# Kernel tuning notes

Measured on AMD Instinct MI355X. Metric: run time of the kernel, lower is better.

## Reference

```python
import jax, jax.numpy as jnp
import numpy as np
import math

NUM_LABELS = 8
D_MODEL = 1024
NUM_HEADS = 16
D_PADDED = math.ceil(D_MODEL / NUM_HEADS) * NUM_HEADS  # 1024
D_HEAD = D_PADDED // NUM_HEADS  # 64
B, N = 4, 2048


def setup_inputs() -> dict:
    key = jax.random.key(0)
    ks = jax.random.split(key, 7)
    X = jax.random.normal(ks[0], (B, N, D_MODEL), dtype=jnp.float32)
    L = jax.random.randint(ks[1], (B, N), 0, NUM_LABELS, dtype=jnp.int32)
    # per-label QKV linear params (stored as x @ W + b layout)
    s_in = 1.0 / math.sqrt(D_MODEL)
    Wqkv = jax.random.uniform(ks[2], (NUM_LABELS, D_MODEL, 3 * D_PADDED), jnp.float32, -s_in, s_in)
    bqkv = jax.random.uniform(ks[3], (NUM_LABELS, 3 * D_PADDED), jnp.float32, -s_in, s_in)
    s_p = 1.0 / math.sqrt(D_PADDED)
    Wproj = jax.random.uniform(ks[4], (D_PADDED, D_MODEL), jnp.float32, -s_p, s_p)
    bproj = jax.random.uniform(ks[5], (D_MODEL,), jnp.float32, -s_p, s_p)
    return {"X": X, "L": L, "Wqkv": Wqkv, "bqkv": bqkv, "Wproj": Wproj, "bproj": bproj}


def reference(X, L, Wqkv, bqkv, Wproj, bproj):
    Bb, Nn, _ = X.shape
    # Per-label dense QKV projection, routed by label mask (matches original
    # per-label loop; X_masked zeroing is a no-op on selected positions).
    qkv = jnp.zeros((Bb, Nn, 3 * D_PADDED), dtype=X.dtype)
    for l in range(NUM_LABELS):
        m = (L == l)[..., None]  # [B, N, 1]
        qkv_l = jnp.einsum('bnd,do->bno', X, Wqkv[l]) + bqkv[l]
        qkv = jnp.where(m, qkv_l, qkv)
    q, k, v = jnp.split(qkv, 3, axis=-1)
    # [B, H, N, Dh]
    q = q.reshape(Bb, Nn, NUM_HEADS, D_HEAD).transpose(0, 2, 1, 3)
    k = k.reshape(Bb, Nn, NUM_HEADS, D_HEAD).transpose(0, 2, 1, 3)
    v = v.reshape(Bb, Nn, NUM_HEADS, D_HEAD).transpose(0, 2, 1, 3)
    scores = jnp.einsum('bhnd,bhmd->bhnm', q, k) / math.sqrt(D_HEAD)
    probs = jax.nn.softmax(scores, axis=-1)
    out = jnp.einsum('bhnm,bhmd->bhnd', probs, v)
    out = out.transpose(0, 2, 1, 3).reshape(Bb, Nn, D_PADDED)
    return jnp.einsum('bnd,do->bno', out, Wproj) + bproj
```

## Files before the change

kernel.cpp:

```cpp
#include <hip/hip_runtime.h>
#include <math.h>

#define BATCH 4
#define SEQ   2048
#define TOK   (BATCH * SEQ)
#define DM    1024
#define DP    1024
#define NH    16
#define DH    64
#define NLAB  8
#define QKV_C 3072
#define PADL  1152
#define PROWS (NLAB * PADL)
#define GP    72

typedef __attribute__((ext_vector_type(8))) short bf16x8;
typedef __attribute__((ext_vector_type(4))) float f32x4;

__device__ __forceinline__ short f2bf(float f) {
  union { float f; unsigned u; } v; v.f = f;
  unsigned r = v.u + 0x7FFF + ((v.u >> 16) & 1);
  return (short)(r >> 16);
}

__device__ __forceinline__ unsigned cvt_pk_bf16(float lo, float hi) {
  unsigned r;
  asm("v_cvt_pk_bf16_f32 %0, %1, %2" : "=v"(r) : "v"(lo), "v"(hi));
  return r;
}

__device__ __forceinline__ float fast_exp2(float x) {
#if __has_builtin(__builtin_amdgcn_exp2f)
  return __builtin_amdgcn_exp2f(x);
#else
  return exp2f(x);
#endif
}

__global__ void build_lists_k(const int* __restrict__ L, int* __restrict__ sorted,
                              int* __restrict__ rowmap) {
  __shared__ int cnt[NLAB], off[NLAB], cur[NLAB];
  int tid = threadIdx.x;
  if (tid < NLAB) cnt[tid] = 0;
  __syncthreads();
  for (int i = tid; i < TOK; i += 256) atomicAdd(&cnt[L[i]], 1);
  __syncthreads();
  if (tid == 0) {
    int o = 0;
    for (int l = 0; l < NLAB; ++l) { off[l] = o; cur[l] = o; o += cnt[l]; }
  }
  __syncthreads();
  for (int i = tid; i < TOK; i += 256) {
    int l = L[i];
    sorted[atomicAdd(&cur[l], 1)] = i;
  }
  __threadfence();
  __syncthreads();
  for (int p = tid; p < PROWS; p += 256) {
    int l = p / PADL, i = p - l * PADL;
    rowmap[p] = (i < cnt[l]) ? sorted[off[l] + i] : -1;
  }
}

__global__ __launch_bounds__(256) void wt_k(const float* __restrict__ src,
                                            short* __restrict__ dst,
                                            int K, int N) {
  __shared__ float Ts[64][65];
  int m = blockIdx.z;
  src += (size_t)m * K * N;
  dst += (size_t)m * (size_t)N * K;
  int n0 = blockIdx.x * 64, k0 = blockIdx.y * 64;
  int tid = threadIdx.x;
  int r = tid >> 4;
  int c = (tid & 15) << 2;
  #pragma unroll
  for (int it = 0; it < 4; ++it) {
    float4 v = *(const float4*)(src + (size_t)(k0 + r + it * 16) * N + n0 + c);
    Ts[c + 0][r + it * 16] = v.x;
    Ts[c + 1][r + it * 16] = v.y;
    Ts[c + 2][r + it * 16] = v.z;
    Ts[c + 3][r + it * 16] = v.w;
  }
  __syncthreads();
  int n = tid >> 2, ks = (tid & 3) << 4;
  short tmp[16];
  #pragma unroll
  for (int j = 0; j < 16; ++j) tmp[j] = f2bf(Ts[n][ks + j]);
  *(bf16x8*)(dst + (size_t)(n0 + n) * K + k0 + ks)     = *(bf16x8*)&tmp[0];
  *(bf16x8*)(dst + (size_t)(n0 + n) * K + k0 + ks + 8) = *(bf16x8*)&tmp[8];
}

__global__ __launch_bounds__(256) void qkv_mfma_k(
    const float* __restrict__ X, const short* __restrict__ Wt,
    const float* __restrict__ bqkv, const int* __restrict__ rowmap,
    short* __restrict__ qkvb) {
  __shared__ short As[128 * GP];
  __shared__ short Bs[128 * GP];
  int bx = blockIdx.x, by = blockIdx.y;
  int lab = by / 9;
  int pr0 = by * 128;
  int n0  = bx * 128;
  const short* W = Wt + (size_t)lab * QKV_C * DM;

  int tid  = threadIdx.x;
  int lane = tid & 63, w = tid >> 6;
  int wm = w >> 1, wn = w & 1;
  int col = lane & 15, quad = lane >> 4;

  int srow = tid >> 2;
  int scol = (tid & 3) << 4;

  int tokA0 = rowmap[pr0 + srow];
  int tokA1 = rowmap[pr0 + 64 + srow];
  const float* xr0 = (tokA0 >= 0) ? (X + (size_t)tokA0 * DM) : nullptr;
  const float* xr1 = (tokA1 >= 0) ? (X + (size_t)tokA1 * DM) : nullptr;

  f32x4 acc[4][4];
  #pragma unroll
  for (int mi = 0; mi < 4; ++mi)
    #pragma unroll
    for (int ni = 0; ni < 4; ++ni) acc[mi][ni] = (f32x4){0.f, 0.f, 0.f, 0.f};

  for (int k0 = 0; k0 < DM; k0 += 64) {
    #pragma unroll
    for (int rep = 0; rep < 2; ++rep) {
      const float* xr = rep ? xr1 : xr0;
      int row = srow + rep * 64;
      short tmp[16];
      if (xr) {
        #pragma unroll
        for (int q4 = 0; q4 < 4; ++q4) {
          float4 v = *(const float4*)(xr + k0 + scol + q4 * 4);
          tmp[q4 * 4 + 0] = f2bf(v.x);
          tmp[q4 * 4 + 1] = f2bf(v.y);
          tmp[q4 * 4 + 2] = f2bf(v.z);
          tmp[q4 * 4 + 3] = f2bf(v.w);
        }
      } else {
        #pragma unroll
        for (int j = 0; j < 16; ++j) tmp[j] = 0;
      }
      *(bf16x8*)&As[row * GP + scol]     = *(bf16x8*)&tmp[0];
      *(bf16x8*)&As[row * GP + scol + 8] = *(bf16x8*)&tmp[8];
    }
    #pragma unroll
    for (int rep = 0; rep < 2; ++rep) {
      int row = srow + rep * 64;
      const short* wsrc = W + (size_t)(n0 + row) * DM + k0 + scol;
      *(bf16x8*)&Bs[row * GP + scol]     = *(const bf16x8*)(wsrc);
      *(bf16x8*)&Bs[row * GP + scol + 8] = *(const bf16x8*)(wsrc + 8);
    }
    __syncthreads();
    #pragma unroll
    for (int ks = 0; ks < 2; ++ks) {
      bf16x8 a[4], b[4];
      #pragma unroll
      for (int mi = 0; mi < 4; ++mi)
        a[mi] = *(bf16x8*)&As[(wm * 64 + mi * 16 + col) * GP + ks * 32 + (quad << 3)];
      #pragma unroll
      for (int ni = 0; ni < 4; ++ni)
        b[ni] = *(bf16x8*)&Bs[(wn * 64 + ni * 16 + col) * GP + ks * 32 + (quad << 3)];
      #pragma unroll
      for (int mi = 0; mi < 4; ++mi)
        #pragma unroll
        for (int ni = 0; ni < 4; ++ni)
          acc[mi][ni] = __builtin_amdgcn_mfma_f32_16x16x32_bf16(a[mi], b[ni], acc[mi][ni], 0, 0, 0);
    }
    __syncthreads();
  }

  float scale = (bx < 8) ? (0.125f * 1.44269504f) : 1.0f;
  const float* bias = bqkv + lab * QKV_C;
  #pragma unroll
  for (int mi = 0; mi < 4; ++mi) {
    #pragma unroll
    for (int r = 0; r < 4; ++r) {
      int prow = pr0 + wm * 64 + mi * 16 + (quad << 2) + r;
      int t2 = rowmap[prow];
      if (t2 < 0) continue;
      #pragma unroll
      for (int ni = 0; ni < 4; ++ni) {
        int gn = n0 + wn * 64 + ni * 16 + col;
        float v = (acc[mi][ni][r] + bias[gn]) * scale;
        qkvb[(size_t)t2 * QKV_C + gn] = f2bf(v);
      }
    }
  }
}

__global__ __launch_bounds__(256) void vtb_k(const short* __restrict__ qkvb,
                                             short* __restrict__ VTg) {
  __shared__ short T[64 * GP];
  int n0 = blockIdx.x * 64, h = blockIdx.y, b = blockIdx.z;
  int tid = threadIdx.x;
  int r = tid >> 2, cb = tid & 3;
  {
    const short* src = qkvb + ((size_t)(b * SEQ + n0 + r)) * QKV_C + 2 * DP + h * DH + (cb << 4);
    int scc = ((cb + (r >> 4)) & 3) << 4;
    *(bf16x8*)&T[r * GP + scc]     = *(const bf16x8*)(src);
    *(bf16x8*)&T[r * GP + scc + 8] = *(const bf16x8*)(src + 8);
  }
  __syncthreads();
  int d = tid >> 2, nc = (tid & 3) << 4;
  int sc2 = (((d >> 4) + (nc >> 4)) & 3) << 4;
  short tmp[16];
  #pragma unroll
  for (int j = 0; j < 16; ++j) tmp[j] = T[(nc + j) * GP + sc2 + (d & 15)];
  short* dst = VTg + ((size_t)(b * NH + h) * DH + d) * SEQ + n0 + nc;
  *(bf16x8*)&dst[0] = *(bf16x8*)&tmp[0];
  *(bf16x8*)&dst[8] = *(bf16x8*)&tmp[8];
}

__global__ __launch_bounds__(256) void attn_k(short* __restrict__ qkvb,
                                              const short* __restrict__ VTg) {
  int qt = blockIdx.x, h = blockIdx.y, b = blockIdx.z;
  __shared__ short Ks[64 * GP];
  __shared__ short VT[64 * GP];
  __shared__ short Ps[128 * GP];

  int tid  = threadIdx.x;
  int lane = tid & 63;
  int w    = tid >> 6;
  int col  = lane & 15;
  int quad = lane >> 4;

  size_t rowbase = (size_t)b * SEQ;
  int hoff = h * DH;
  int sr = tid >> 2;
  int sc = (tid & 3) << 4;

  const short* ksrc = qkvb + (rowbase + sr) * QKV_C + DP + hoff + sc;
  const short* vsrc = VTg + ((size_t)(b * NH + h) * DH + sr) * SEQ + sc;

  bf16x8 qf0[2], qf1[2];
  {
    const short* q0 = qkvb + (rowbase + qt * 128 + (w << 4) + col) * QKV_C + hoff + (quad << 3);
    const short* q1 = q0 + (size_t)64 * QKV_C;
    qf0[0] = *(const bf16x8*)(q0);
    qf0[1] = *(const bf16x8*)(q0 + 32);
    qf1[0] = *(const bf16x8*)(q1);
    qf1[1] = *(const bf16x8*)(q1 + 32);
  }

  {
    bf16x8 ka = *(const bf16x8*)(ksrc);
    bf16x8 kb = *(const bf16x8*)(ksrc + 8);
    bf16x8 va = *(const bf16x8*)(vsrc);
    bf16x8 vb = *(const bf16x8*)(vsrc + 8);
    *(bf16x8*)&Ks[sr * GP + sc]     = ka;
    *(bf16x8*)&Ks[sr * GP + sc + 8] = kb;
    *(bf16x8*)&VT[sr * GP + sc]     = va;
    *(bf16x8*)&VT[sr * GP + sc + 8] = vb;
  }
  __syncthreads();

  float m_0 = -1e30f, l_0 = 0.f, m_1 = -1e30f, l_1 = 0.f;
  f32x4 o0[4], o1[4];
  #pragma unroll
  for (int nd = 0; nd < 4; ++nd) {
    o0[nd] = (f32x4){0.f, 0.f, 0.f, 0.f};
    o1[nd] = (f32x4){0.f, 0.f, 0.f, 0.f};
  }

  short* ps0 = &Ps[((w << 4) + col) * GP];
  short* ps1 = &Ps[(64 + (w << 4) + col) * GP];

  auto softmax_strip = [&](f32x4* s, float& m_, float& l_, f32x4* o, short* psrow) {
    f32x4 t0, t1;
    #pragma unroll
    for (int i = 0; i < 4; ++i) { t0[i] = fmaxf(s[0][i], s[1][i]); t1[i] = fmaxf(s[2][i], s[3][i]); }
    #pragma unroll
    for (int i = 0; i < 4; ++i) t0[i] = fmaxf(t0[i], t1[i]);
    float mx = fmaxf(fmaxf(t0[0], t0[1]), fmaxf(t0[2], t0[3]));
    mx = fmaxf(mx, __shfl_xor(mx, 16));
    mx = fmaxf(mx, __shfl_xor(mx, 32));
    float mnew  = fmaxf(m_, mx);
    float alpha = fast_exp2(m_ - mnew);
    float p[4][4];
    #pragma unroll
    for (int nj = 0; nj < 4; ++nj)
      #pragma unroll
      for (int r = 0; r < 4; ++r) p[nj][r] = fast_exp2(s[nj][r] - mnew);
    float rs = 0.f;
    #pragma unroll
    for (int nj = 0; nj < 4; ++nj)
      rs += (p[nj][0] + p[nj][1]) + (p[nj][2] + p[nj][3]);
    rs += __shfl_xor(rs, 16);
    rs += __shfl_xor(rs, 32);
    l_ = l_ * alpha + rs;
    m_ = mnew;
    #pragma unroll
    for (int nd = 0; nd < 4; ++nd)
      #pragma unroll
      for (int r = 0; r < 4; ++r) o[nd][r] *= alpha;
    #pragma unroll
    for (int nj = 0; nj < 4; ++nj) {
      uint2 u;
      u.x = cvt_pk_bf16(p[nj][0], p[nj][1]);
      u.y = cvt_pk_bf16(p[nj][2], p[nj][3]);
      *(uint2*)&psrow[nj * 16 + (quad << 2)] = u;
    }
  };

  auto compute_tile = [&]() {
    f32x4 s0[4], s1[4];
    #pragma unroll
    for (int nj = 0; nj < 4; ++nj) {
      s0[nj] = (f32x4){0.f, 0.f, 0.f, 0.f};
      s1[nj] = (f32x4){0.f, 0.f, 0.f, 0.f};
    }
    #pragma unroll
    for (int ks = 0; ks < 2; ++ks) {
      #pragma unroll
      for (int nj = 0; nj < 4; ++nj) {
        bf16x8 aK = *(bf16x8*)&Ks[((nj << 4) + col) * GP + (ks << 5) + (quad << 3)];
        s0[nj] = __builtin_amdgcn_mfma_f32_16x16x32_bf16(aK, qf0[ks], s0[nj], 0, 0, 0);
        s1[nj] = __builtin_amdgcn_mfma_f32_16x16x32_bf16(aK, qf1[ks], s1[nj], 0, 0, 0);
      }
    }
    softmax_strip(s0, m_0, l_0, o0, ps0);
    softmax_strip(s1, m_1, l_1, o1, ps1);
    #pragma unroll
    for (int ks = 0; ks < 2; ++ks) {
      bf16x8 bP0 = *(bf16x8*)&ps0[(ks << 5) + (quad << 3)];
      bf16x8 bP1 = *(bf16x8*)&ps1[(ks << 5) + (quad << 3)];
      #pragma unroll
      for (int nd = 0; nd < 4; ++nd) {
        bf16x8 aV = *(bf16x8*)&VT[((nd << 4) + col) * GP + (ks << 5) + (quad << 3)];
        o0[nd] = __builtin_amdgcn_mfma_f32_16x16x32_bf16(aV, bP0, o0[nd], 0, 0, 0);
        o1[nd] = __builtin_amdgcn_mfma_f32_16x16x32_bf16(aV, bP1, o1[nd], 0, 0, 0);
      }
    }
  };

  for (int kt = 0; kt < SEQ / 64 - 1; ++kt) {
    const short* kn = ksrc + (size_t)(kt + 1) * 64 * QKV_C;
    const short* vn = vsrc + (size_t)(kt + 1) * 64;
    bf16x8 ka = *(const bf16x8*)(kn);
    bf16x8 kb = *(const bf16x8*)(kn + 8);
    bf16x8 va = *(const bf16x8*)(vn);
    bf16x8 vb = *(const bf16x8*)(vn + 8);

    compute_tile();
    __syncthreads();
    *(bf16x8*)&Ks[sr * GP + sc]     = ka;
    *(bf16x8*)&Ks[sr * GP + sc + 8] = kb;
    *(bf16x8*)&VT[sr * GP + sc]     = va;
    *(bf16x8*)&VT[sr * GP + sc + 8] = vb;
    __syncthreads();
  }
  compute_tile();

  #pragma unroll
  for (int s = 0; s < 2; ++s) {
    float inv = 1.f / (s ? l_1 : l_0);
    f32x4* o = s ? o1 : o0;
    size_t row = rowbase + qt * 128 + s * 64 + (w << 4) + col;
    #pragma unroll
    for (int nd = 0; nd < 4; ++nd) {
      uint2 u;
      u.x = cvt_pk_bf16(o[nd][0] * inv, o[nd][1] * inv);
      u.y = cvt_pk_bf16(o[nd][2] * inv, o[nd][3] * inv);
      *(uint2*)(qkvb + row * QKV_C + hoff + (nd << 4) + (quad << 2)) = u;
    }
  }
}

__global__ __launch_bounds__(256) void proj_mfma_k(
    const short* __restrict__ Ab, const short* __restrict__ Wt,
    const float* __restrict__ bias, float* __restrict__ out) {
  __shared__ short As[128 * GP];
  __shared__ short Bs[128 * GP];
  int n0 = blockIdx.x * 128, m0 = blockIdx.y * 128;

  int tid  = threadIdx.x;
  int lane = tid & 63, w = tid >> 6;
  int wm = w >> 1, wn = w & 1;
  int col = lane & 15, quad = lane >> 4;
  int srow = tid >> 2;
  int scol = (tid & 3) << 4;

  f32x4 acc[4][4];
  #pragma unroll
  for (int mi = 0; mi < 4; ++mi)
    #pragma unroll
    for (int ni = 0; ni < 4; ++ni) acc[mi][ni] = (f32x4){0.f, 0.f, 0.f, 0.f};

  for (int k0 = 0; k0 < DP; k0 += 64) {
    #pragma unroll
    for (int rep = 0; rep < 2; ++rep) {
      int row = srow + rep * 64;
      const short* asrc = Ab + (size_t)(m0 + row) * QKV_C + k0 + scol;
      *(bf16x8*)&As[row * GP + scol]     = *(const bf16x8*)(asrc);
      *(bf16x8*)&As[row * GP + scol + 8] = *(const bf16x8*)(asrc + 8);
      const short* wsrc = Wt + (size_t)(n0 + row) * DP + k0 + scol;
      *(bf16x8*)&Bs[row * GP + scol]     = *(const bf16x8*)(wsrc);
      *(bf16x8*)&Bs[row * GP + scol + 8] = *(const bf16x8*)(wsrc + 8);
    }
    __syncthreads();
    #pragma unroll
    for (int ks = 0; ks < 2; ++ks) {
      bf16x8 a[4], b[4];
      #pragma unroll
      for (int mi = 0; mi < 4; ++mi)
        a[mi] = *(bf16x8*)&As[(wm * 64 + mi * 16 + col) * GP + ks * 32 + (quad << 3)];
      #pragma unroll
      for (int ni = 0; ni < 4; ++ni)
        b[ni] = *(bf16x8*)&Bs[(wn * 64 + ni * 16 + col) * GP + ks * 32 + (quad << 3)];
      #pragma unroll
      for (int mi = 0; mi < 4; ++mi)
        #pragma unroll
        for (int ni = 0; ni < 4; ++ni)
          acc[mi][ni] = __builtin_amdgcn_mfma_f32_16x16x32_bf16(a[mi], b[ni], acc[mi][ni], 0, 0, 0);
    }
    __syncthreads();
  }

  #pragma unroll
  for (int mi = 0; mi < 4; ++mi) {
    #pragma unroll
    for (int r = 0; r < 4; ++r) {
      int m = m0 + wm * 64 + mi * 16 + (quad << 2) + r;
      #pragma unroll
      for (int ni = 0; ni < 4; ++ni) {
        int gn = n0 + wn * 64 + ni * 16 + col;
        out[(size_t)m * DM + gn] = acc[mi][ni][r] + bias[gn];
      }
    }
  }
}

extern "C" void kernel_launch(void* const* d_in, const int* in_sizes, int n_in,
                              void* d_out, int out_size, void* d_ws, size_t ws_size,
                              hipStream_t stream) {
  (void)in_sizes; (void)n_in; (void)out_size; (void)ws_size;
  const float* X     = (const float*)d_in[0];
  const int*   L     = (const int*)d_in[1];
  const float* Wqkv  = (const float*)d_in[2];
  const float* bqkv  = (const float*)d_in[3];
  const float* Wproj = (const float*)d_in[4];
  const float* bproj = (const float*)d_in[5];
  float* out = (float*)d_out;

  char* ws = (char*)d_ws;
  short* qkvb    = (short*)ws;
  short* Wqkv_t  = (short*)(ws + (size_t)TOK * QKV_C * 2);
  short* Wproj_t = (short*)(ws + (size_t)TOK * QKV_C * 2
                               + (size_t)NLAB * QKV_C * DM * 2);
  int* sorted = (int*)((char*)Wproj_t + (size_t)DP * DM * 2);
  int* rowmap = sorted + TOK;
  short* VTg = Wqkv_t;

  build_lists_k<<<dim3(1), dim3(256), 0, stream>>>(L, sorted, rowmap);
  wt_k<<<dim3(QKV_C / 64, DM / 64, NLAB), dim3(256), 0, stream>>>(Wqkv, Wqkv_t, DM, QKV_C);
  wt_k<<<dim3(DM / 64, DP / 64, 1), dim3(256), 0, stream>>>(Wproj, Wproj_t, DP, DM);
  qkv_mfma_k<<<dim3(QKV_C / 128, PROWS / 128), dim3(256), 0, stream>>>(
      X, Wqkv_t, bqkv, rowmap, qkvb);
  vtb_k<<<dim3(SEQ / 64, NH, BATCH), dim3(256), 0, stream>>>(qkvb, VTg);
  attn_k<<<dim3(SEQ / 128, NH, BATCH), dim3(256), 0, stream>>>(qkvb, VTg);
  proj_mfma_k<<<dim3(DM / 128, TOK / 128), dim3(256), 0, stream>>>(
      qkvb, Wproj_t, bproj, out);
}
```

Measured before the change: 542.5 us.

## Pre-gather X to bf16 and register-prefetch next K tile in GEMMs

Adds a gather kernel that writes label-sorted X rows as bf16 into a padded buffer, so the QKV GEMM no longer does per-tile fp32 loads, bf16 conversion and row indirection repeated across 24 column blocks. Both the QKV and projection GEMMs now prefetch the next K tile into registers after the barrier, so global loads overlap the MFMA work. The cost is an extra kernel launch, an extra bf16 buffer in the workspace, and higher register pressure.

Result: faster. 476.9 us (-12.1%).

```diff
diff --git a/kernel.cpp b/kernel.cpp
--- a/kernel.cpp
+++ b/kernel.cpp
@@ -62,6 +62,23 @@
   }
 }
 
+__global__ __launch_bounds__(256) void xg_k(const float* __restrict__ X,
+                                            const int* __restrict__ rowmap,
+                                            short* __restrict__ Xg) {
+  int p = blockIdx.x;
+  int t = rowmap[p];
+  int c = threadIdx.x << 2;
+  short* dst = Xg + (size_t)p * DM + c;
+  if (t >= 0) {
+    float4 v = *(const float4*)(X + (size_t)t * DM + c);
+    short tmp[4] = { f2bf(v.x), f2bf(v.y), f2bf(v.z), f2bf(v.w) };
+    *(uint2*)dst = *(uint2*)tmp;
+  } else {
+    uint2 z; z.x = 0u; z.y = 0u;
+    *(uint2*)dst = z;
+  }
+}
+
 __global__ __launch_bounds__(256) void wt_k(const float* __restrict__ src,
                                             short* __restrict__ dst,
                                             int K, int N) {
@@ -91,7 +108,7 @@
 }
 
 __global__ __launch_bounds__(256) void qkv_mfma_k(
-    const float* __restrict__ X, const short* __restrict__ Wt,
+    const short* __restrict__ Xg, const short* __restrict__ Wt,
     const float* __restrict__ bqkv, const int* __restrict__ rowmap,
     short* __restrict__ qkvb) {
   __shared__ short As[128 * GP];
@@ -110,10 +127,10 @@
   int srow = tid >> 2;
   int scol = (tid & 3) << 4;
 
-  int tokA0 = rowmap[pr0 + srow];
-  int tokA1 = rowmap[pr0 + 64 + srow];
-  const float* xr0 = (tokA0 >= 0) ? (X + (size_t)tokA0 * DM) : nullptr;
-  const float* xr1 = (tokA1 >= 0) ? (X + (size_t)tokA1 * DM) : nullptr;
+  const short* a0 = Xg + (size_t)(pr0 + srow) * DM + scol;
+  const short* a1 = Xg + (size_t)(pr0 + 64 + srow) * DM + scol;
+  const short* b0 = W + (size_t)(n0 + srow) * DM + scol;
+  const short* b1 = W + (size_t)(n0 + 64 + srow) * DM + scol;
 
   f32x4 acc[4][4];
   #pragma unroll
@@ -121,36 +138,29 @@
     #pragma unroll
     for (int ni = 0; ni < 4; ++ni) acc[mi][ni] = (f32x4){0.f, 0.f, 0.f, 0.f};
 
+  bf16x8 ra[4], rb[4];
+  ra[0] = *(const bf16x8*)(a0);     ra[1] = *(const bf16x8*)(a0 + 8);
+  ra[2] = *(const bf16x8*)(a1);     ra[3] = *(const bf16x8*)(a1 + 8);
+  rb[0] = *(const bf16x8*)(b0);     rb[1] = *(const bf16x8*)(b0 + 8);
+  rb[2] = *(const bf16x8*)(b1);     rb[3] = *(const bf16x8*)(b1 + 8);
+
   for (int k0 = 0; k0 < DM; k0 += 64) {
-    #pragma unroll
-    for (int rep = 0; rep < 2; ++rep) {
-      const float* xr = rep ? xr1 : xr0;
-      int row = srow + rep * 64;
-      short tmp[16];
-      if (xr) {
-        #pragma unroll
-        for (int q4 = 0; q4 < 4; ++q4) {
-          float4 v = *(const float4*)(xr + k0 + scol + q4 * 4);
-          tmp[q4 * 4 + 0] = f2bf(v.x);
-          tmp[q4 * 4 + 1] = f2bf(v.y);
-          tmp[q4 * 4 + 2] = f2bf(v.z);
-          tmp[q4 * 4 + 3] = f2bf(v.w);
-        }
-      } else {
-        #pragma unroll
-        for (int j = 0; j < 16; ++j) tmp[j] = 0;
-      }
-      *(bf16x8*)&As[row * GP + scol]     = *(bf16x8*)&tmp[0];
-      *(bf16x8*)&As[row * GP + scol + 8] = *(bf16x8*)&tmp[8];
-    }
-    #pragma unroll
-    for (int rep = 0; rep < 2; ++rep) {
-      int row = srow + rep * 64;
-      const short* wsrc = W + (size_t)(n0 + row) * DM + k0 + scol;
-      *(bf16x8*)&Bs[row * GP + scol]     = *(const bf16x8*)(wsrc);
-      *(bf16x8*)&Bs[row * GP + scol + 8] = *(const bf16x8*)(wsrc + 8);
-    }
-    __syncthreads();
+    *(bf16x8*)&As[srow * GP + scol]            = ra[0];
+    *(bf16x8*)&As[srow * GP + scol + 8]        = ra[1];
+    *(bf16x8*)&As[(64 + srow) * GP + scol]     = ra[2];
+    *(bf16x8*)&As[(64 + srow) * GP + scol + 8] = ra[3];
+    *(bf16x8*)&Bs[srow * GP + scol]            = rb[0];
+    *(bf16x8*)&Bs[srow * GP + scol + 8]        = rb[1];
+    *(bf16x8*)&Bs[(64 + srow) * GP + scol]     = rb[2];
+    *(bf16x8*)&Bs[(64 + srow) * GP + scol + 8] = rb[3];
+    __syncthreads();
+    if (k0 + 64 < DM) {
+      int kn = k0 + 64;
+      ra[0] = *(const bf16x8*)(a0 + kn);     ra[1] = *(const bf16x8*)(a0 + kn + 8);
+      ra[2] = *(const bf16x8*)(a1 + kn);     ra[3] = *(const bf16x8*)(a1 + kn + 8);
+      rb[0] = *(const bf16x8*)(b0 + kn);     rb[1] = *(const bf16x8*)(b0 + kn + 8);
+      rb[2] = *(const bf16x8*)(b1 + kn);     rb[3] = *(const bf16x8*)(b1 + kn + 8);
+    }
     #pragma unroll
     for (int ks = 0; ks < 2; ++ks) {
       bf16x8 a[4], b[4];
@@ -380,24 +390,40 @@
   int srow = tid >> 2;
   int scol = (tid & 3) << 4;
 
+  const short* a0 = Ab + (size_t)(m0 + srow) * QKV_C + scol;
+  const short* a1 = Ab + (size_t)(m0 + 64 + srow) * QKV_C + scol;
+  const short* b0 = Wt + (size_t)(n0 + srow) * DP + scol;
+  const short* b1 = Wt + (size_t)(n0 + 64 + srow) * DP + scol;
+
   f32x4 acc[4][4];
   #pragma unroll
   for (int mi = 0; mi < 4; ++mi)
     #pragma unroll
     for (int ni = 0; ni < 4; ++ni) acc[mi][ni] = (f32x4){0.f, 0.f, 0.f, 0.f};
 
+  bf16x8 ra[4], rb[4];
+  ra[0] = *(const bf16x8*)(a0);     ra[1] = *(const bf16x8*)(a0 + 8);
+  ra[2] = *(const bf16x8*)(a1);     ra[3] = *(const bf16x8*)(a1 + 8);
+  rb[0] = *(const bf16x8*)(b0);     rb[1] = *(const bf16x8*)(b0 + 8);
+  rb[2] = *(const bf16x8*)(b1);     rb[3] = *(const bf16x8*)(b1 + 8);
+
   for (int k0 = 0; k0 < DP; k0 += 64) {
-    #pragma unroll
-    for (int rep = 0; rep < 2; ++rep) {
-      int row = srow + rep * 64;
-      const short* asrc = Ab + (size_t)(m0 + row) * QKV_C + k0 + scol;
-      *(bf16x8*)&As[row * GP + scol]     = *(const bf16x8*)(asrc);
-      *(bf16x8*)&As[row * GP + scol + 8] = *(const bf16x8*)(asrc + 8);
-      const short* wsrc = Wt + (size_t)(n0 + row) * DP + k0 + scol;
-      *(bf16x8*)&Bs[row * GP + scol]     = *(const bf16x8*)(wsrc);
-      *(bf16x8*)&Bs[row * GP + scol + 8] = *(const bf16x8*)(wsrc + 8);
-    }
-    __syncthreads();
+    *(bf16x8*)&As[srow * GP + scol]            = ra[0];
+    *(bf16x8*)&As[srow * GP + scol + 8]        = ra[1];
+    *(bf16x8*)&As[(64 + srow) * GP + scol]     = ra[2];
+    *(bf16x8*)&As[(64 + srow) * GP + scol + 8] = ra[3];
+    *(bf16x8*)&Bs[srow * GP + scol]            = rb[0];
+    *(bf16x8*)&Bs[srow * GP + scol + 8]        = rb[1];
+    *(bf16x8*)&Bs[(64 + srow) * GP + scol]     = rb[2];
+    *(bf16x8*)&Bs[(64 + srow) * GP + scol + 8] = rb[3];
+    __syncthreads();
+    if (k0 + 64 < DP) {
+      int kn = k0 + 64;
+      ra[0] = *(const bf16x8*)(a0 + kn);     ra[1] = *(const bf16x8*)(a0 + kn + 8);
+      ra[2] = *(const bf16x8*)(a1 + kn);     ra[3] = *(const bf16x8*)(a1 + kn + 8);
+      rb[0] = *(const bf16x8*)(b0 + kn);     rb[1] = *(const bf16x8*)(b0 + kn + 8);
+      rb[2] = *(const bf16x8*)(b1 + kn);     rb[3] = *(const bf16x8*)(b1 + kn + 8);
+    }
     #pragma unroll
     for (int ks = 0; ks < 2; ++ks) {
       bf16x8 a[4], b[4];
@@ -449,13 +475,15 @@
                                + (size_t)NLAB * QKV_C * DM * 2);
   int* sorted = (int*)((char*)Wproj_t + (size_t)DP * DM * 2);
   int* rowmap = sorted + TOK;
+  short* Xg = (short*)(rowmap + PROWS);
   short* VTg = Wqkv_t;
 
   build_lists_k<<<dim3(1), dim3(256), 0, stream>>>(L, sorted, rowmap);
+  xg_k<<<dim3(PROWS), dim3(256), 0, stream>>>(X, rowmap, Xg);
   wt_k<<<dim3(QKV_C / 64, DM / 64, NLAB), dim3(256), 0, stream>>>(Wqkv, Wqkv_t, DM, QKV_C);
   wt_k<<<dim3(DM / 64, DP / 64, 1), dim3(256), 0, stream>>>(Wproj, Wproj_t, DP, DM);
   qkv_mfma_k<<<dim3(QKV_C / 128, PROWS / 128), dim3(256), 0, stream>>>(
-      X, Wqkv_t, bqkv, rowmap, qkvb);
+      Xg, Wqkv_t, bqkv, rowmap, qkvb);
   vtb_k<<<dim3(SEQ / 64, NH, BATCH), dim3(256), 0, stream>>>(qkvb, VTg);
   attn_k<<<dim3(SEQ / 128, NH, BATCH), dim3(256), 0, stream>>>(qkvb, VTg);
   proj_mfma_k<<<dim3(DM / 128, TOK / 128), dim3(256), 0, stream>>>(
```
